# Performance work log

Measured on AMD Instinct MI355X. Metric: run time of the kernel, lower is better.

Reference implementation:

```python
import jax, jax.numpy as jnp
import numpy as np

B, L, F, H = 8, 1024, 1024, 16
D = F // H  # feat_head = 64
EPS = 1e-5


def setup_inputs() -> dict:
    key = jax.random.key(0)
    ks = jax.random.split(key, 12)
    s = 1.0 / np.sqrt(F)
    inp = {
        "q": jax.random.normal(ks[0], (B, L, F), jnp.float32),
        "k": jax.random.normal(ks[1], (B, L, F), jnp.float32),
        "v": jax.random.normal(ks[2], (B, L, F), jnp.float32),
        "Wq": jax.random.uniform(ks[3], (F, F), jnp.float32, -s, s),
        "bq": jax.random.uniform(ks[4], (F,), jnp.float32, -s, s),
        "Wk": jax.random.uniform(ks[5], (F, F), jnp.float32, -s, s),
        "bk": jax.random.uniform(ks[6], (F,), jnp.float32, -s, s),
        "Wv": jax.random.uniform(ks[7], (F, F), jnp.float32, -s, s),
        "bv": jax.random.uniform(ks[8], (F,), jnp.float32, -s, s),
        "Wf": jax.random.uniform(ks[9], (F, F), jnp.float32, -s, s),
        "bf": jax.random.uniform(ks[10], (F,), jnp.float32, -s, s),
        "gamma": jnp.ones((F,), jnp.float32),
        "beta": jnp.zeros((F,), jnp.float32),
    }
    return inp


def _split_heads(x):
    # (B, L, F) -> (B*H, L, D), matching reshape->transpose(1,2)->reshape
    return x.reshape(B, L, H, D).transpose(0, 2, 1, 3).reshape(B * H, L, D)


def reference(q, k, v, Wq, bq, Wk, bk, Wv, bv, Wf, bf, gamma, beta):
    residual = q
    qh = _split_heads(q @ Wq.T + bq)
    kh = _split_heads(k @ Wk.T + bk)
    vh = _split_heads(v @ Wv.T + bv)
    # scores: (B*H, L, L)
    scores = jnp.einsum('nqd,nkd->nqk', qh, kh) / np.sqrt(D)
    raw_att = jax.nn.softmax(scores, axis=-1)
    att = jnp.einsum('nqk,nkd->nqd', raw_att, vh)  # (B*H, L, D)
    # faithful to original output recombine: reshape(H, B, L, D).permute(1,2,0,3)
    att = att.reshape(H, B, L, D).transpose(1, 2, 0, 3).reshape(B, L, F)
    att = att @ Wf.T + bf
    # dropout in eval mode = identity; activation is None
    x = att + residual
    mu = jnp.mean(x, axis=-1, keepdims=True)
    var = jnp.mean(jnp.square(x - mu), axis=-1, keepdims=True)
    out = (x - mu) * jax.lax.rsqrt(var + EPS) * gamma + beta
    return out, raw_att
```

## Files before the change

### kernel.cpp

```cpp
#include <hip/hip_runtime.h>

#define BB 8
#define LL 1024
#define FF 1024
#define HH 16
#define DD 64
#define NBH 128

typedef __attribute__((ext_vector_type(8))) short bf16x8;
typedef __attribute__((ext_vector_type(4))) float f32x4;

#define GLD_LDS16(g, l)                                                        \
  __builtin_amdgcn_global_load_lds(                                            \
      (const __attribute__((address_space(1))) unsigned int*)(g),              \
      (__attribute__((address_space(3))) unsigned int*)(l), 16, 0, 0)

__device__ __forceinline__ unsigned short f2bf(float f) {
  unsigned int u = __float_as_uint(f);
  unsigned int r = u + 0x7fffu + ((u >> 16) & 1u);
  return (unsigned short)(r >> 16);
}
__device__ __forceinline__ float bf2f(unsigned short s) {
  return __uint_as_float(((unsigned int)s) << 16);
}

__global__ __launch_bounds__(256) void cvt3_kernel(const float* __restrict__ s0,
                                                   const float* __restrict__ s1,
                                                   const float* __restrict__ s2,
                                                   short* __restrict__ dst, int n4) {
  int z = blockIdx.y;
  const float* src = (z == 0) ? s0 : (z == 1) ? s1 : s2;
  int i = blockIdx.x * 256 + threadIdx.x;
  if (i >= n4) return;
  float4 v = ((const float4*)src)[i];
  short4 o;
  o.x = (short)f2bf(v.x); o.y = (short)f2bf(v.y);
  o.z = (short)f2bf(v.z); o.w = (short)f2bf(v.w);
  ((short4*)(dst + (size_t)z * n4 * 4))[i] = o;
}

__global__ __launch_bounds__(256) void cvt4_kernel(const float* __restrict__ s0,
                                                   const float* __restrict__ s1,
                                                   const float* __restrict__ s2,
                                                   const float* __restrict__ s3,
                                                   short* __restrict__ dst, int n4) {
  int z = blockIdx.y;
  const float* src = (z == 0) ? s0 : (z == 1) ? s1 : (z == 2) ? s2 : s3;
  int i = blockIdx.x * 256 + threadIdx.x;
  if (i >= n4) return;
  float4 v = ((const float4*)src)[i];
  short4 o;
  o.x = (short)f2bf(v.x); o.y = (short)f2bf(v.y);
  o.z = (short)f2bf(v.z); o.w = (short)f2bf(v.w);
  ((short4*)(dst + (size_t)z * n4 * 4))[i] = o;
}

__global__ __launch_bounds__(256) void proj_qkv(
    const short* __restrict__ Aall, const short* __restrict__ Wall,
    const float* __restrict__ bq, const float* __restrict__ bk,
    const float* __restrict__ bv, short* __restrict__ Dall) {
  const int o = blockIdx.x + (blockIdx.y << 6) + (blockIdx.z << 9);
  const int n = ((o & 7) * 192) + (o >> 3);
  const int z = n >> 9;
  const int r = n & 511;
  const int by = r & 7, bx = r >> 3;

  const short* A  = Aall + (size_t)z * (BB * LL * FF);
  const short* Bt = Wall + (size_t)z * (FF * FF);
  const float* bias = (z == 0) ? bq : (z == 1) ? bk : bv;
  short* dst = Dall + (size_t)z * ((size_t)NBH * LL * DD);
  const float scale = (z == 0) ? 0.125f * 1.44269504088896f : 1.0f;

  __shared__ __attribute__((aligned(16))) short LB[128 * 136];
  short* As = LB;
  short* Bs = LB + 128 * 64;

  const int tid = threadIdx.x;
  const int lane = tid & 63, w = tid >> 6;
  const int wr = w >> 1, wc = w & 1;
  const int row16 = lane & 15, kg = lane >> 4;
  const int m0 = bx * 128, n0 = by * 128;

  const f32x4 z4 = {0.f, 0.f, 0.f, 0.f};
  f32x4 acc[4][4];
  for (int i = 0; i < 4; ++i)
    for (int j = 0; j < 4; ++j) acc[i][j] = z4;

  for (int k0 = 0; k0 < FF; k0 += 64) {
#pragma unroll
    for (int rr = 0; rr < 4; ++rr) {
      int e8 = tid + rr * 256;
      int row = e8 >> 3, cs = ((e8 & 7) ^ (row & 7)) * 8;
      GLD_LDS16(A + (size_t)(m0 + row) * FF + k0 + cs, As + e8 * 8);
      GLD_LDS16(Bt + (size_t)(n0 + row) * FF + k0 + cs, Bs + e8 * 8);
    }
    __syncthreads();
#pragma unroll
    for (int kk2 = 0; kk2 < 2; ++kk2) {
      bf16x8 af[4], bfr[4];
#pragma unroll
      for (int i = 0; i < 4; ++i) {
        int ra = wr * 64 + i * 16 + row16;
        int rb = wc * 64 + i * 16 + row16;
        af[i]  = *(const bf16x8*)(As + ra * 64 + ((((kk2 << 2) | kg) ^ (ra & 7)) << 3));
        bfr[i] = *(const bf16x8*)(Bs + rb * 64 + ((((kk2 << 2) | kg) ^ (rb & 7)) << 3));
      }
#pragma unroll
      for (int i = 0; i < 4; ++i)
#pragma unroll
        for (int j = 0; j < 4; ++j)
          acc[i][j] = __builtin_amdgcn_mfma_f32_16x16x32_bf16(af[i], bfr[j], acc[i][j], 0, 0, 0);
    }
    __syncthreads();
  }

  const int z2 = (z == 2);
#pragma unroll
  for (int i = 0; i < 4; ++i) {
#pragma unroll
    for (int j = 0; j < 4; ++j) {
      int nl = wc * 64 + j * 16 + row16;
      float bn = bias[n0 + nl];
#pragma unroll
      for (int rr = 0; rr < 4; ++rr) {
        int ml = wr * 64 + i * 16 + kg * 4 + rr;
        float val = (acc[i][j][rr] + bn) * scale;
        int rrow = z2 ? nl : ml, ccol = z2 ? ml : nl;
        LB[rrow * 136 + ccol] = (short)f2bf(val);
      }
    }
  }
  __syncthreads();
  const int b = m0 >> 10;
  const int lbase = m0 & 1023;
#pragma unroll
  for (int rr = 0; rr < 8; ++rr) {
    int e = tid + rr * 256;
    int row = e >> 4, c8 = e & 15;
    uint4 val = *(const uint4*)(LB + row * 136 + c8 * 8);
    if (!z2) {
      int l = lbase + row;
      int h = (n0 + c8 * 8) >> 6, d = (c8 & 7) * 8;
      *(uint4*)(dst + (((size_t)(b * HH + h)) * LL + l) * DD + d) = val;
    } else {
      int h = (n0 + row) >> 6, d = (n0 + row) & 63;
      int l = lbase + c8 * 8;
      *(uint4*)(dst + (((size_t)(b * HH + h)) * DD + d) * LL + l) = val;
    }
  }
}

__global__ __launch_bounds__(256) void attn_kernel(
    const short* __restrict__ Qh, const short* __restrict__ Kh,
    const short* __restrict__ Vt, float* __restrict__ Patt,
    short* __restrict__ attb) {
  const int o = blockIdx.x + (blockIdx.y << 4);
  const int n = ((o & 7) << 8) + (o >> 3);
  const int bh = n >> 4;
  const int q0 = (n & 15) * 64;
  const int tid = threadIdx.x;
  const int lane = tid & 63, w = tid >> 6;
  const int row16 = lane & 15, kg = lane >> 4;

  __shared__ __attribute__((aligned(16))) short Qs[64 * 64];
  __shared__ __attribute__((aligned(16))) short Ks[2][64 * 64];
  __shared__ __attribute__((aligned(16))) short Vts[2][64 * 64];
  __shared__ __attribute__((aligned(16))) short PsT[4][16 * 64];

  auto kbuf3 = [&](int i) -> short* {
    return (i == 2) ? &Vts[0][0] : &Ks[i][0];
  };

#define STAGE_K(tt, dstp)                                                      \
  {                                                                            \
    int e8a = tid, rowa = e8a >> 3, c8a = (e8a & 7) ^ (rowa & 7);              \
    GLD_LDS16(Kh + ((size_t)bh * LL + (tt) * 64 + rowa) * DD + c8a * 8,        \
              (dstp) + e8a * 8);                                               \
    int e8b = tid + 256, rowb = e8b >> 3, c8b = (e8b & 7) ^ (rowb & 7);        \
    GLD_LDS16(Kh + ((size_t)bh * LL + (tt) * 64 + rowb) * DD + c8b * 8,        \
              (dstp) + e8b * 8);                                               \
  }
#define STAGE_V(tt, dstp)                                                      \
  {                                                                            \
    int e8a = tid, rowa = e8a >> 3, c8a = (e8a & 7) ^ (rowa & 7);              \
    GLD_LDS16(Vt + ((size_t)bh * DD + rowa) * LL + (tt) * 64 + c8a * 8,        \
              (dstp) + e8a * 8);                                               \
    int e8b = tid + 256, rowb = e8b >> 3, c8b = (e8b & 7) ^ (rowb & 7);        \
    GLD_LDS16(Vt + ((size_t)bh * DD + rowb) * LL + (tt) * 64 + c8b * 8,        \
              (dstp) + e8b * 8);                                               \
  }

  {
    int e8a = tid, rowa = e8a >> 3, c8a = (e8a & 7) ^ (rowa & 7);
    GLD_LDS16(Qh + ((size_t)bh * LL + q0 + rowa) * DD + c8a * 8, Qs + e8a * 8);
    int e8b = tid + 256, rowb = e8b >> 3, c8b = (e8b & 7) ^ (rowb & 7);
    GLD_LDS16(Qh + ((size_t)bh * LL + q0 + rowb) * DD + c8b * 8, Qs + e8b * 8);
  }
  STAGE_K(0, kbuf3(0));
  STAGE_K(1, kbuf3(1));
  asm volatile("s_waitcnt vmcnt(2)" ::: "memory");
  __builtin_amdgcn_s_barrier();

  const int qrow = w * 16 + row16;
  bf16x8 aq0 = *(const bf16x8*)(Qs + qrow * 64 + ((kg ^ (qrow & 7)) << 3));
  bf16x8 aq1 = *(const bf16x8*)(Qs + qrow * 64 + (((kg + 4) ^ (qrow & 7)) << 3));

  const f32x4 z4 = {0.f, 0.f, 0.f, 0.f};
  float lsum = 0.f;

  for (int t = 0; t < 16; ++t) {
    const short* kb = kbuf3(t % 3);
    if (t < 14) {
      short* kd = kbuf3((t + 2) % 3);
      STAGE_K(t + 2, kd);
    }
    f32x4 s[4] = {z4, z4, z4, z4};
    __builtin_amdgcn_s_setprio(1);
#pragma unroll
    for (int tt = 0; tt < 4; ++tt) {
      int krow = tt * 16 + row16;
      bf16x8 b0 = *(const bf16x8*)(kb + krow * 64 + ((kg ^ (krow & 7)) << 3));
      bf16x8 b1 = *(const bf16x8*)(kb + krow * 64 + (((kg + 4) ^ (krow & 7)) << 3));
      s[tt] = __builtin_amdgcn_mfma_f32_16x16x32_bf16(b0, aq0, s[tt], 0, 0, 0);
      s[tt] = __builtin_amdgcn_mfma_f32_16x16x32_bf16(b1, aq1, s[tt], 0, 0, 0);
    }
    __builtin_amdgcn_s_setprio(0);
#pragma unroll
    for (int tt = 0; tt < 4; ++tt)
#pragma unroll
      for (int rr = 0; rr < 4; ++rr) lsum += exp2f(s[tt][rr]);
    if (t < 14) {
      asm volatile("s_waitcnt vmcnt(2)" ::: "memory");
    } else {
      asm volatile("s_waitcnt vmcnt(0)" ::: "memory");
    }
    __builtin_amdgcn_s_barrier();
  }
  lsum += __shfl_xor(lsum, 16);
  lsum += __shfl_xor(lsum, 32);
  const float lc = __log2f(lsum);

  f32x4 oT[4] = {z4, z4, z4, z4};

  STAGE_K(0, &Ks[0][0]);
  STAGE_V(0, &Vts[0][0]);
  asm volatile("s_waitcnt vmcnt(0)" ::: "memory");
  __builtin_amdgcn_s_barrier();
  for (int t = 0; t < 16; ++t) {
    const int cur = t & 1;
    if (t < 15) {
      STAGE_K(t + 1, &Ks[cur ^ 1][0]);
      STAGE_V(t + 1, &Vts[cur ^ 1][0]);
    }
    f32x4 s[4] = {z4, z4, z4, z4};
    __builtin_amdgcn_s_setprio(1);
#pragma unroll
    for (int tt = 0; tt < 4; ++tt) {
      int krow = tt * 16 + row16;
      bf16x8 b0 = *(const bf16x8*)(&Ks[cur][krow * 64 + ((kg ^ (krow & 7)) << 3)]);
      bf16x8 b1 = *(const bf16x8*)(&Ks[cur][krow * 64 + (((kg + 4) ^ (krow & 7)) << 3)]);
      s[tt] = __builtin_amdgcn_mfma_f32_16x16x32_bf16(b0, aq0, s[tt], 0, 0, 0);
      s[tt] = __builtin_amdgcn_mfma_f32_16x16x32_bf16(b1, aq1, s[tt], 0, 0, 0);
    }
    __builtin_amdgcn_s_setprio(0);
    const int qq = q0 + w * 16 + row16;
    const int k0 = t * 64;
#pragma unroll
    for (int tt = 0; tt < 4; ++tt) {
      f32x4 pv;
#pragma unroll
      for (int rr = 0; rr < 4; ++rr) pv[rr] = exp2f(s[tt][rr] - lc);
      __builtin_nontemporal_store(
          pv, (f32x4*)(Patt + ((size_t)bh * LL + qq) * LL + k0 + tt * 16 + kg * 4));
      short4 ps;
      ps.x = (short)f2bf(pv[0]); ps.y = (short)f2bf(pv[1]);
      ps.z = (short)f2bf(pv[2]); ps.w = (short)f2bf(pv[3]);
      int c = ((tt * 2 + (kg >> 1)) ^ (row16 & 7));
      *(short4*)(&PsT[w][row16 * 64 + c * 8 + (kg & 1) * 4]) = ps;
    }
    bf16x8 pb0 = *(const bf16x8*)(&PsT[w][row16 * 64 + ((kg ^ (row16 & 7)) << 3)]);
    bf16x8 pb1 = *(const bf16x8*)(&PsT[w][row16 * 64 + (((4 + kg) ^ (row16 & 7)) << 3)]);
    __builtin_amdgcn_s_setprio(1);
#pragma unroll
    for (int td = 0; td < 4; ++td) {
      int trow = td * 16 + row16;
      bf16x8 v0 = *(const bf16x8*)(&Vts[cur][trow * 64 + ((kg ^ (trow & 7)) << 3)]);
      bf16x8 v1 = *(const bf16x8*)(&Vts[cur][trow * 64 + (((kg + 4) ^ (trow & 7)) << 3)]);
      oT[td] = __builtin_amdgcn_mfma_f32_16x16x32_bf16(v0, pb0, oT[td], 0, 0, 0);
      oT[td] = __builtin_amdgcn_mfma_f32_16x16x32_bf16(v1, pb1, oT[td], 0, 0, 0);
    }
    __builtin_amdgcn_s_setprio(0);
    if (t < 15) {
      asm volatile("s_waitcnt vmcnt(4)" ::: "memory");
      __builtin_amdgcn_s_barrier();
    }
  }

  const int iblk = bh >> 3;
  const int jb = bh & 7;
  const int qq = q0 + w * 16 + row16;
#pragma unroll
  for (int td = 0; td < 4; ++td) {
    short4 ov;
    ov.x = (short)f2bf(oT[td][0]); ov.y = (short)f2bf(oT[td][1]);
    ov.z = (short)f2bf(oT[td][2]); ov.w = (short)f2bf(oT[td][3]);
    *(short4*)(attb + ((size_t)jb * LL + qq) * FF + iblk * 64 + td * 16 + kg * 4) = ov;
  }
#undef STAGE_K
#undef STAGE_V
}

__global__ __launch_bounds__(256) void proj_out(
    const short* __restrict__ A, const short* __restrict__ Bt,
    const float* __restrict__ bias, const short* __restrict__ resid,
    short* __restrict__ xb) {
  const int o = blockIdx.x + (blockIdx.y << 6);
  const int n = ((o & 7) << 6) + (o >> 3);
  const int by = n & 7, bx = n >> 3;

  __shared__ __attribute__((aligned(16))) short As[128 * 64];
  __shared__ __attribute__((aligned(16))) short Bs[128 * 64];

  const int tid = threadIdx.x;
  const int lane = tid & 63, w = tid >> 6;
  const int wr = w >> 1, wc = w & 1;
  const int row16 = lane & 15, kg = lane >> 4;
  const int m0 = bx * 128, n0 = by * 128;

  const f32x4 z4 = {0.f, 0.f, 0.f, 0.f};
  f32x4 acc[4][4];
  for (int i = 0; i < 4; ++i)
    for (int j = 0; j < 4; ++j) acc[i][j] = z4;

  for (int k0 = 0; k0 < FF; k0 += 64) {
#pragma unroll
    for (int rr = 0; rr < 4; ++rr) {
      int e8 = tid + rr * 256;
      int row = e8 >> 3, cs = ((e8 & 7) ^ (row & 7)) * 8;
      GLD_LDS16(A + (size_t)(m0 + row) * FF + k0 + cs, As + e8 * 8);
      GLD_LDS16(Bt + (size_t)(n0 + row) * FF + k0 + cs, Bs + e8 * 8);
    }
    __syncthreads();
#pragma unroll
    for (int kk2 = 0; kk2 < 2; ++kk2) {
      bf16x8 af[4], bfr[4];
#pragma unroll
      for (int i = 0; i < 4; ++i) {
        int ra = wr * 64 + i * 16 + row16;
        int rb = wc * 64 + i * 16 + row16;
        af[i]  = *(const bf16x8*)(As + ra * 64 + ((((kk2 << 2) | kg) ^ (ra & 7)) << 3));
        bfr[i] = *(const bf16x8*)(Bs + rb * 64 + ((((kk2 << 2) | kg) ^ (rb & 7)) << 3));
      }
#pragma unroll
      for (int i = 0; i < 4; ++i)
#pragma unroll
        for (int j = 0; j < 4; ++j)
          acc[i][j] = __builtin_amdgcn_mfma_f32_16x16x32_bf16(af[i], bfr[j], acc[i][j], 0, 0, 0);
    }
    __syncthreads();
  }

#pragma unroll
  for (int i = 0; i < 4; ++i) {
#pragma unroll
    for (int j = 0; j < 4; ++j) {
      int ncol = n0 + wc * 64 + j * 16 + row16;
      float bn = bias[ncol];
#pragma unroll
      for (int rr = 0; rr < 4; ++rr) {
        int m = m0 + wr * 64 + i * 16 + kg * 4 + rr;
        float val = acc[i][j][rr] + bn + bf2f((unsigned short)resid[(size_t)m * FF + ncol]);
        xb[(size_t)m * FF + ncol] = (short)f2bf(val);
      }
    }
  }
}

__global__ __launch_bounds__(256) void ln_kernel(const short* __restrict__ xb,
                                                 const float* __restrict__ gamma,
                                                 const float* __restrict__ beta,
                                                 float* __restrict__ out) {
  const int row = blockIdx.x;
  const int tid = threadIdx.x;
  const short4 v4 = *(const short4*)(xb + (size_t)row * FF + tid * 4);
  float vx = bf2f((unsigned short)v4.x), vy = bf2f((unsigned short)v4.y);
  float vz = bf2f((unsigned short)v4.z), vw = bf2f((unsigned short)v4.w);
  float s = vx + vy + vz + vw;
  float s2 = vx * vx + vy * vy + vz * vz + vw * vw;
#pragma unroll
  for (int o = 1; o < 64; o <<= 1) {
    s += __shfl_xor(s, o);
    s2 += __shfl_xor(s2, o);
  }
  __shared__ float ss[4], ss2[4];
  int w = tid >> 6, lane = tid & 63;
  if (lane == 0) { ss[w] = s; ss2[w] = s2; }
  __syncthreads();
  s = ss[0] + ss[1] + ss[2] + ss[3];
  s2 = ss2[0] + ss2[1] + ss2[2] + ss2[3];
  float mu = s * (1.0f / 1024.0f);
  float var = s2 * (1.0f / 1024.0f) - mu * mu;
  float rs = rsqrtf(var + 1e-5f);
  float4 g = *(const float4*)(gamma + tid * 4);
  float4 be = *(const float4*)(beta + tid * 4);
  float4 o;
  o.x = (vx - mu) * rs * g.x + be.x;
  o.y = (vy - mu) * rs * g.y + be.y;
  o.z = (vz - mu) * rs * g.z + be.z;
  o.w = (vw - mu) * rs * g.w + be.w;
  *(float4*)(out + (size_t)row * FF + tid * 4) = o;
}

extern "C" void kernel_launch(void* const* d_in, const int* in_sizes, int n_in,
                              void* d_out, int out_size, void* d_ws, size_t ws_size,
                              hipStream_t stream) {
  const float* q  = (const float*)d_in[0];
  const float* k  = (const float*)d_in[1];
  const float* v  = (const float*)d_in[2];
  const float* Wq = (const float*)d_in[3];
  const float* bq = (const float*)d_in[4];
  const float* Wk = (const float*)d_in[5];
  const float* bk = (const float*)d_in[6];
  const float* Wv = (const float*)d_in[7];
  const float* bv = (const float*)d_in[8];
  const float* Wf = (const float*)d_in[9];
  const float* bf = (const float*)d_in[10];
  const float* gamma = (const float*)d_in[11];
  const float* beta  = (const float*)d_in[12];

  float* out = (float*)d_out;
  float* Patt = out + (size_t)BB * LL * FF;

  char* ws = (char*)d_ws;
  const size_t MB = (size_t)1 << 20;
  short* qb = (short*)(ws + 0 * MB);
  short* Wb = (short*)(ws + 48 * MB);
  short* Qh = (short*)(ws + 56 * MB);
  short* Kh = (short*)(ws + 72 * MB);
  short* Vt = (short*)(ws + 88 * MB);
  short* attb = (short*)(ws + 32 * MB);
  short* xb = (short*)(ws + 16 * MB);

  const int nAct4 = BB * LL * FF / 4;
  const int nW4 = FF * FF / 4;
  cvt3_kernel<<<dim3((nAct4 + 255) / 256, 3), 256, 0, stream>>>(q, k, v, qb, nAct4);
  cvt4_kernel<<<dim3((nW4 + 255) / 256, 4), 256, 0, stream>>>(Wq, Wk, Wv, Wf, Wb, nW4);

  proj_qkv<<<dim3(64, 8, 3), 256, 0, stream>>>(qb, Wb, bq, bk, bv, Qh);
  attn_kernel<<<dim3(16, 128), 256, 0, stream>>>(Qh, Kh, Vt, Patt, attb);
  proj_out<<<dim3(64, 8), 256, 0, stream>>>(attb, Wb + 3 * (size_t)FF * FF, bf, qb, xb);
  ln_kernel<<<8192, 256, 0, stream>>>(xb, gamma, beta, out);
}
```

Measured before the change: 289.0 us.

## Process 128 query rows per attention block to reuse K/V tiles

After: 329.2 us. 13.9% more time.

```diff
diff --git a/kernel.cpp b/kernel.cpp
--- a/kernel.cpp
+++ b/kernel.cpp
@@ -154,18 +154,18 @@
     const short* __restrict__ Qh, const short* __restrict__ Kh,
     const short* __restrict__ Vt, float* __restrict__ Patt,
     short* __restrict__ attb) {
-  const int o = blockIdx.x + (blockIdx.y << 4);
-  const int n = ((o & 7) << 8) + (o >> 3);
-  const int bh = n >> 4;
-  const int q0 = (n & 15) * 64;
+  const int o = blockIdx.x + (blockIdx.y << 3);
+  const int n = ((o & 7) << 7) + (o >> 3);
+  const int bh = n >> 3;
+  const int q0 = (n & 7) * 128;
   const int tid = threadIdx.x;
   const int lane = tid & 63, w = tid >> 6;
   const int row16 = lane & 15, kg = lane >> 4;
 
-  __shared__ __attribute__((aligned(16))) short Qs[64 * 64];
+  __shared__ __attribute__((aligned(16))) short Qs[128 * 64];
   __shared__ __attribute__((aligned(16))) short Ks[2][64 * 64];
   __shared__ __attribute__((aligned(16))) short Vts[2][64 * 64];
-  __shared__ __attribute__((aligned(16))) short PsT[4][16 * 64];
+  __shared__ __attribute__((aligned(16))) short PsT[4][2][16 * 64];
 
   auto kbuf3 = [&](int i) -> short* {
     return (i == 2) ? &Vts[0][0] : &Ks[i][0];
@@ -191,22 +191,27 @@
   }
 
   {
-    int e8a = tid, rowa = e8a >> 3, c8a = (e8a & 7) ^ (rowa & 7);
-    GLD_LDS16(Qh + ((size_t)bh * LL + q0 + rowa) * DD + c8a * 8, Qs + e8a * 8);
-    int e8b = tid + 256, rowb = e8b >> 3, c8b = (e8b & 7) ^ (rowb & 7);
-    GLD_LDS16(Qh + ((size_t)bh * LL + q0 + rowb) * DD + c8b * 8, Qs + e8b * 8);
+#pragma unroll
+    for (int r = 0; r < 4; ++r) {
+      int e8 = tid + r * 256;
+      int row = e8 >> 3, c8 = (e8 & 7) ^ (row & 7);
+      GLD_LDS16(Qh + ((size_t)bh * LL + q0 + row) * DD + c8 * 8, Qs + e8 * 8);
+    }
   }
   STAGE_K(0, kbuf3(0));
   STAGE_K(1, kbuf3(1));
   asm volatile("s_waitcnt vmcnt(2)" ::: "memory");
   __builtin_amdgcn_s_barrier();
 
-  const int qrow = w * 16 + row16;
-  bf16x8 aq0 = *(const bf16x8*)(Qs + qrow * 64 + ((kg ^ (qrow & 7)) << 3));
-  bf16x8 aq1 = *(const bf16x8*)(Qs + qrow * 64 + (((kg + 4) ^ (qrow & 7)) << 3));
+  const int qrA = w * 16 + row16;
+  const int qrB = qrA + 64;
+  bf16x8 aqA0 = *(const bf16x8*)(Qs + qrA * 64 + ((kg ^ (qrA & 7)) << 3));
+  bf16x8 aqA1 = *(const bf16x8*)(Qs + qrA * 64 + (((kg + 4) ^ (qrA & 7)) << 3));
+  bf16x8 aqB0 = *(const bf16x8*)(Qs + qrB * 64 + ((kg ^ (qrB & 7)) << 3));
+  bf16x8 aqB1 = *(const bf16x8*)(Qs + qrB * 64 + (((kg + 4) ^ (qrB & 7)) << 3));
 
   const f32x4 z4 = {0.f, 0.f, 0.f, 0.f};
-  float lsum = 0.f;
+  float lsumA = 0.f, lsumB = 0.f;
 
   for (int t = 0; t < 16; ++t) {
     const short* kb = kbuf3(t % 3);
@@ -214,21 +219,35 @@
       short* kd = kbuf3((t + 2) % 3);
       STAGE_K(t + 2, kd);
     }
-    f32x4 s[4] = {z4, z4, z4, z4};
+    f32x4 s[4];
     __builtin_amdgcn_s_setprio(1);
 #pragma unroll
     for (int tt = 0; tt < 4; ++tt) {
       int krow = tt * 16 + row16;
       bf16x8 b0 = *(const bf16x8*)(kb + krow * 64 + ((kg ^ (krow & 7)) << 3));
       bf16x8 b1 = *(const bf16x8*)(kb + krow * 64 + (((kg + 4) ^ (krow & 7)) << 3));
-      s[tt] = __builtin_amdgcn_mfma_f32_16x16x32_bf16(b0, aq0, s[tt], 0, 0, 0);
-      s[tt] = __builtin_amdgcn_mfma_f32_16x16x32_bf16(b1, aq1, s[tt], 0, 0, 0);
+      s[tt] = __builtin_amdgcn_mfma_f32_16x16x32_bf16(b0, aqA0, z4, 0, 0, 0);
+      s[tt] = __builtin_amdgcn_mfma_f32_16x16x32_bf16(b1, aqA1, s[tt], 0, 0, 0);
     }
     __builtin_amdgcn_s_setprio(0);
 #pragma unroll
     for (int tt = 0; tt < 4; ++tt)
 #pragma unroll
-      for (int rr = 0; rr < 4; ++rr) lsum += exp2f(s[tt][rr]);
+      for (int rr = 0; rr < 4; ++rr) lsumA += exp2f(s[tt][rr]);
+    __builtin_amdgcn_s_setprio(1);
+#pragma unroll
+    for (int tt = 0; tt < 4; ++tt) {
+      int krow = tt * 16 + row16;
+      bf16x8 b0 = *(const bf16x8*)(kb + krow * 64 + ((kg ^ (krow & 7)) << 3));
+      bf16x8 b1 = *(const bf16x8*)(kb + krow * 64 + (((kg + 4) ^ (krow & 7)) << 3));
+      s[tt] = __builtin_amdgcn_mfma_f32_16x16x32_bf16(b0, aqB0, z4, 0, 0, 0);
+      s[tt] = __builtin_amdgcn_mfma_f32_16x16x32_bf16(b1, aqB1, s[tt], 0, 0, 0);
+    }
+    __builtin_amdgcn_s_setprio(0);
+#pragma unroll
+    for (int tt = 0; tt < 4; ++tt)
+#pragma unroll
+      for (int rr = 0; rr < 4; ++rr) lsumB += exp2f(s[tt][rr]);
     if (t < 14) {
       asm volatile("s_waitcnt vmcnt(2)" ::: "memory");
     } else {
@@ -236,75 +255,110 @@
     }
     __builtin_amdgcn_s_barrier();
   }
-  lsum += __shfl_xor(lsum, 16);
-  lsum += __shfl_xor(lsum, 32);
-  const float lc = __log2f(lsum);
-
-  f32x4 oT[4] = {z4, z4, z4, z4};
+  lsumA += __shfl_xor(lsumA, 16);
+  lsumA += __shfl_xor(lsumA, 32);
+  lsumB += __shfl_xor(lsumB, 16);
+  lsumB += __shfl_xor(lsumB, 32);
+  const float lcA = __log2f(lsumA);
+  const float lcB = __log2f(lsumB);
+
+  f32x4 oTA[4] = {z4, z4, z4, z4};
+  f32x4 oTB[4] = {z4, z4, z4, z4};
 
   STAGE_K(0, &Ks[0][0]);
   STAGE_V(0, &Vts[0][0]);
   asm volatile("s_waitcnt vmcnt(0)" ::: "memory");
   __builtin_amdgcn_s_barrier();
+  const int qqA = q0 + qrA;
+  const int qqB = q0 + qrB;
   for (int t = 0; t < 16; ++t) {
     const int cur = t & 1;
     if (t < 15) {
       STAGE_K(t + 1, &Ks[cur ^ 1][0]);
       STAGE_V(t + 1, &Vts[cur ^ 1][0]);
     }
-    f32x4 s[4] = {z4, z4, z4, z4};
+    const int k0 = t * 64;
+    f32x4 s[4];
     __builtin_amdgcn_s_setprio(1);
 #pragma unroll
     for (int tt = 0; tt < 4; ++tt) {
       int krow = tt * 16 + row16;
       bf16x8 b0 = *(const bf16x8*)(&Ks[cur][krow * 64 + ((kg ^ (krow & 7)) << 3)]);
       bf16x8 b1 = *(const bf16x8*)(&Ks[cur][krow * 64 + (((kg + 4) ^ (krow & 7)) << 3)]);
-      s[tt] = __builtin_amdgcn_mfma_f32_16x16x32_bf16(b0, aq0, s[tt], 0, 0, 0);
-      s[tt] = __builtin_amdgcn_mfma_f32_16x16x32_bf16(b1, aq1, s[tt], 0, 0, 0);
+      s[tt] = __builtin_amdgcn_mfma_f32_16x16x32_bf16(b0, aqA0, z4, 0, 0, 0);
+      s[tt] = __builtin_amdgcn_mfma_f32_16x16x32_bf16(b1, aqA1, s[tt], 0, 0, 0);
     }
     __builtin_amdgcn_s_setprio(0);
-    const int qq = q0 + w * 16 + row16;
-    const int k0 = t * 64;
 #pragma unroll
     for (int tt = 0; tt < 4; ++tt) {
       f32x4 pv;
 #pragma unroll
-      for (int rr = 0; rr < 4; ++rr) pv[rr] = exp2f(s[tt][rr] - lc);
+      for (int rr = 0; rr < 4; ++rr) pv[rr] = exp2f(s[tt][rr] - lcA);
       __builtin_nontemporal_store(
-          pv, (f32x4*)(Patt + ((size_t)bh * LL + qq) * LL + k0 + tt * 16 + kg * 4));
+          pv, (f32x4*)(Patt + ((size_t)bh * LL + qqA) * LL + k0 + tt * 16 + kg * 4));
       short4 ps;
       ps.x = (short)f2bf(pv[0]); ps.y = (short)f2bf(pv[1]);
       ps.z = (short)f2bf(pv[2]); ps.w = (short)f2bf(pv[3]);
       int c = ((tt * 2 + (kg >> 1)) ^ (row16 & 7));
-      *(short4*)(&PsT[w][row16 * 64 + c * 8 + (kg & 1) * 4]) = ps;
-    }
-    bf16x8 pb0 = *(const bf16x8*)(&PsT[w][row16 * 64 + ((kg ^ (row16 & 7)) << 3)]);
-    bf16x8 pb1 = *(const bf16x8*)(&PsT[w][row16 * 64 + (((4 + kg) ^ (row16 & 7)) << 3)]);
+      *(short4*)(&PsT[w][0][row16 * 64 + c * 8 + (kg & 1) * 4]) = ps;
+    }
+    __builtin_amdgcn_s_setprio(1);
+#pragma unroll
+    for (int tt = 0; tt < 4; ++tt) {
+      int krow = tt * 16 + row16;
+      bf16x8 b0 = *(const bf16x8*)(&Ks[cur][krow * 64 + ((kg ^ (krow & 7)) << 3)]);
+      bf16x8 b1 = *(const bf16x8*)(&Ks[cur][krow * 64 + (((kg + 4) ^ (krow & 7)) << 3)]);
+      s[tt] = __builtin_amdgcn_mfma_f32_16x16x32_bf16(b0, aqB0, z4, 0, 0, 0);
+      s[tt] = __builtin_amdgcn_mfma_f32_16x16x32_bf16(b1, aqB1, s[tt], 0, 0, 0);
+    }
+    __builtin_amdgcn_s_setprio(0);
+#pragma unroll
+    for (int tt = 0; tt < 4; ++tt) {
+      f32x4 pv;
+#pragma unroll
+      for (int rr = 0; rr < 4; ++rr) pv[rr] = exp2f(s[tt][rr] - lcB);
+      __builtin_nontemporal_store(
+          pv, (f32x4*)(Patt + ((size_t)bh * LL + qqB) * LL + k0 + tt * 16 + kg * 4));
+      short4 ps;
+      ps.x = (short)f2bf(pv[0]); ps.y = (short)f2bf(pv[1]);
+      ps.z = (short)f2bf(pv[2]); ps.w = (short)f2bf(pv[3]);
+      int c = ((tt * 2 + (kg >> 1)) ^ (row16 & 7));
+      *(short4*)(&PsT[w][1][row16 * 64 + c * 8 + (kg & 1) * 4]) = ps;
+    }
+    bf16x8 pbA0 = *(const bf16x8*)(&PsT[w][0][row16 * 64 + ((kg ^ (row16 & 7)) << 3)]);
+    bf16x8 pbA1 = *(const bf16x8*)(&PsT[w][0][row16 * 64 + (((4 + kg) ^ (row16 & 7)) << 3)]);
+    bf16x8 pbB0 = *(const bf16x8*)(&PsT[w][1][row16 * 64 + ((kg ^ (row16 & 7)) << 3)]);
+    bf16x8 pbB1 = *(const bf16x8*)(&PsT[w][1][row16 * 64 + (((4 + kg) ^ (row16 & 7)) << 3)]);
     __builtin_amdgcn_s_setprio(1);
 #pragma unroll
     for (int td = 0; td < 4; ++td) {
       int trow = td * 16 + row16;
       bf16x8 v0 = *(const bf16x8*)(&Vts[cur][trow * 64 + ((kg ^ (trow & 7)) << 3)]);
       bf16x8 v1 = *(const bf16x8*)(&Vts[cur][trow * 64 + (((kg + 4) ^ (trow & 7)) << 3)]);
-      oT[td] = __builtin_amdgcn_mfma_f32_16x16x32_bf16(v0, pb0, oT[td], 0, 0, 0);
-      oT[td] = __builtin_amdgcn_mfma_f32_16x16x32_bf16(v1, pb1, oT[td], 0, 0, 0);
+      oTA[td] = __builtin_amdgcn_mfma_f32_16x16x32_bf16(v0, pbA0, oTA[td], 0, 0, 0);
+      oTA[td] = __builtin_amdgcn_mfma_f32_16x16x32_bf16(v1, pbA1, oTA[td], 0, 0, 0);
+      oTB[td] = __builtin_amdgcn_mfma_f32_16x16x32_bf16(v0, pbB0, oTB[td], 0, 0, 0);
+      oTB[td] = __builtin_amdgcn_mfma_f32_16x16x32_bf16(v1, pbB1, oTB[td], 0, 0, 0);
     }
     __builtin_amdgcn_s_setprio(0);
     if (t < 15) {
-      asm volatile("s_waitcnt vmcnt(4)" ::: "memory");
+      asm volatile("s_waitcnt vmcnt(8)" ::: "memory");
       __builtin_amdgcn_s_barrier();
     }
   }
 
   const int iblk = bh >> 3;
   const int jb = bh & 7;
-  const int qq = q0 + w * 16 + row16;
 #pragma unroll
   for (int td = 0; td < 4; ++td) {
     short4 ov;
-    ov.x = (short)f2bf(oT[td][0]); ov.y = (short)f2bf(oT[td][1]);
-    ov.z = (short)f2bf(oT[td][2]); ov.w = (short)f2bf(oT[td][3]);
-    *(short4*)(attb + ((size_t)jb * LL + qq) * FF + iblk * 64 + td * 16 + kg * 4) = ov;
+    ov.x = (short)f2bf(oTA[td][0]); ov.y = (short)f2bf(oTA[td][1]);
+    ov.z = (short)f2bf(oTA[td][2]); ov.w = (short)f2bf(oTA[td][3]);
+    *(short4*)(attb + ((size_t)jb * LL + qqA) * FF + iblk * 64 + td * 16 + kg * 4) = ov;
+    short4 ow;
+    ow.x = (short)f2bf(oTB[td][0]); ow.y = (short)f2bf(oTB[td][1]);
+    ow.z = (short)f2bf(oTB[td][2]); ow.w = (short)f2bf(oTB[td][3]);
+    *(short4*)(attb + ((size_t)jb * LL + qqB) * FF + iblk * 64 + td * 16 + kg * 4) = ow;
   }
 #undef STAGE_K
 #undef STAGE_V
@@ -447,7 +501,7 @@
   cvt4_kernel<<<dim3((nW4 + 255) / 256, 4), 256, 0, stream>>>(Wq, Wk, Wv, Wf, Wb, nW4);
 
   proj_qkv<<<dim3(64, 8, 3), 256, 0, stream>>>(qb, Wb, bq, bk, bv, Qh);
-  attn_kernel<<<dim3(16, 128), 256, 0, stream>>>(Qh, Kh, Vt, Patt, attb);
+  attn_kernel<<<dim3(8, 128), 256, 0, stream>>>(Qh, Kh, Vt, Patt, attb);
   proj_out<<<dim3(64, 8), 256, 0, stream>>>(attb, Wb + 3 * (size_t)FF * FF, bf, qb, xb);
   ln_kernel<<<8192, 256, 0, stream>>>(xb, gamma, beta, out);
 }
```
